# Kernel tuning notes

Hardware: AMD Instinct MI355X
Metric: run time of the kernel (lower is better)

The kernel has to match this reference:

```python
import jax, jax.numpy as jnp
import numpy as np

B, C, H, D, W = 1, 32, 32, 32, 32   # batch, channels, 3D grid
M1 = M2 = M3 = 16                   # fourier modes kept per dim
KS = 3                              # spatial attention kernel size
MEM = 5                             # memory slots
EPS = 1e-5
N = H * D * W


def _gelu(x):
    return jax.nn.gelu(x, approximate=False)  # torch exact GELU


def _gn(x):
    # GroupNorm(1, C) without affine: normalize over (C,H,D,W) per sample
    mu = jnp.mean(x, axis=(1, 2, 3, 4), keepdims=True)
    var = jnp.var(x, axis=(1, 2, 3, 4), keepdims=True)
    return (x - mu) * jax.lax.rsqrt(var + EPS)


def _spectral_conv(x, wr, wi):
    # classic 3D FNO spectral conv: keep low modes (4 corner blocks in dims H,D; low block in rfft dim W)
    xf = jnp.fft.rfftn(x, axes=(2, 3, 4))                 # (B,C,H,D,W//2+1) complex64
    w = wr + 1j * wi                                      # (4,Cin,Cout,M1,M2,M3)
    of = jnp.zeros((x.shape[0], C, H, D, W // 2 + 1), xf.dtype)
    corners = [(slice(0, M1), slice(0, M2)), (slice(H - M1, H), slice(0, M2)),
               (slice(0, M1), slice(D - M2, D)), (slice(H - M1, H), slice(D - M2, D))]
    for i, (s1, s2) in enumerate(corners):
        of = of.at[:, :, s1, s2, :M3].set(
            jnp.einsum('bixyz,ioxyz->boxyz', xf[:, :, s1, s2, :M3], w[i]))
    return jnp.fft.irfftn(of, s=(H, D, W), axes=(2, 3, 4))


def _forward(x, t, prev_memory, w_spec_r, w_spec_i, norm1_g, norm1_b,
             mlp_w1, mlp_b1, mlp_w2, mlp_b2, tin_gw, tin_gb, tin_bw, tin_bb,
             q_w, q_b, k_w, k_b, v_w, v_b, mem_key, mem_value,
             gate_w, gate_b, gru_wih, gru_whh, gru_bih, gru_bhh):
    skip1 = x
    skip2 = _gelu(x)
    # spectral conv -> GroupNorm(affine) + residual -> gelu
    h = _spectral_conv(x, w_spec_r, w_spec_i)
    h = _gelu(_gn(h) * norm1_g[None, :, None, None, None]
              + norm1_b[None, :, None, None, None] + skip1)
    # pointwise Conv1d MLP over channels
    hf = h.reshape(B, C, N)
    u = _gelu(jnp.einsum('oc,bcn->bon', mlp_w1, hf) + mlp_b1[None, :, None])
    hf = jnp.einsum('oc,bcn->bon', mlp_w2, u) + mlp_b2[None, :, None]
    h = hf.reshape(B, C, H, D, W)
    # time-conditioned instance norm: gamma/beta from 1x1 conv over t (B,C)
    gamma = (jnp.einsum('oc,bc->bo', tin_gw, t) + tin_gb)[:, :, None, None, None]
    beta = (jnp.einsum('oc,bc->bo', tin_bw, t) + tin_bb)[:, :, None, None, None]
    h = gamma * _gn(h) + beta
    # ---- spatial attention with memory ----
    pad = KS // 2
    xp = jnp.pad(h, ((0, 0), (0, 0), (pad, pad), (pad, pad), (pad, pad)))
    # 3D unfold: (B,C,27,N) patches via 27 shifted views
    patches = jnp.stack([xp[:, :, i:i + H, j:j + D, l:l + W]
                         for i in range(KS) for j in range(KS) for l in range(KS)],
                        axis=2).reshape(B, C, KS ** 3, N)
    hf = h.reshape(B, C, N)
    q = jnp.einsum('oc,bcn->bon', q_w, hf) + q_b[None, :, None]              # (B,C,N)
    k_sp = jnp.einsum('oc,bcmn->bomn', k_w, patches) + k_b[None, :, None, None]
    v_sp = jnp.einsum('oc,bcmn->bomn', v_w, patches) + v_b[None, :, None, None]
    mem_k = jnp.broadcast_to(mem_key[None, :, :, None], (B, C, MEM, N))
    mem_v = jnp.broadcast_to(mem_value[None, :, :, None], (B, C, MEM, N))
    k = jnp.concatenate([mem_k, k_sp], axis=2)                               # (B,C,32,N)
    v = jnp.concatenate([mem_v, v_sp], axis=2)
    attn = jax.nn.softmax(q[:, :, None, :] * k / jnp.sqrt(jnp.float32(C)), axis=2)
    out = jnp.sum(attn * v, axis=2)                                          # (B,C,N)
    cat = jnp.concatenate([hf, out], axis=1)                                 # (B,2C,N)
    gate = jax.nn.sigmoid(jnp.einsum('oc,bcn->bon', gate_w, cat) + gate_b[None, :, None])
    out = gate * out + (1.0 - gate) * hf
    out = out.reshape(B, C, H, D, W)
    # GRUCell memory update from spatially pooled features
    m_in = jnp.mean(out, axis=(2, 3, 4))                                     # (B,C)
    gi = m_in @ gru_wih.T + gru_bih
    gh = prev_memory @ gru_whh.T + gru_bhh
    ir, iz, inn = jnp.split(gi, 3, axis=1)
    hr, hz, hn = jnp.split(gh, 3, axis=1)
    r = jax.nn.sigmoid(ir + hr)
    z = jax.nn.sigmoid(iz + hz)
    n = jnp.tanh(inn + r * hn)
    new_memory = (1.0 - z) * n + z * prev_memory                             # (B,C)
    return out + skip2, new_memory


def setup_inputs():
    key = jax.random.key(0)
    ks = jax.random.split(key, 20)
    def rn(k, shape, s):
        return jax.random.normal(k, shape, jnp.float32) * s
    spec_scale = 1.0 / (C * C)
    return dict(
        x=jax.random.normal(ks[0], (B, C, H, D, W), jnp.float32),
        t=jax.random.normal(ks[1], (B, C), jnp.float32),
        prev_memory=jnp.zeros((B, C), jnp.float32),
        w_spec_r=rn(ks[2], (4, C, C, M1, M2, M3), spec_scale),
        w_spec_i=rn(ks[3], (4, C, C, M1, M2, M3), spec_scale),
        norm1_g=jnp.ones((C,), jnp.float32),
        norm1_b=jnp.zeros((C,), jnp.float32),
        mlp_w1=rn(ks[4], (C // 2, C), 0.1), mlp_b1=jnp.zeros((C // 2,), jnp.float32),
        mlp_w2=rn(ks[5], (C, C // 2), 0.1), mlp_b2=jnp.zeros((C,), jnp.float32),
        tin_gw=rn(ks[6], (C, C), 0.1), tin_gb=jnp.ones((C,), jnp.float32),
        tin_bw=rn(ks[7], (C, C), 0.1), tin_bb=jnp.zeros((C,), jnp.float32),
        q_w=rn(ks[8], (C, C), 0.1), q_b=jnp.zeros((C,), jnp.float32),
        k_w=rn(ks[9], (C, C), 0.1), k_b=jnp.zeros((C,), jnp.float32),
        v_w=rn(ks[10], (C, C), 0.1), v_b=jnp.zeros((C,), jnp.float32),
        mem_key=jax.random.normal(ks[11], (C, MEM), jnp.float32),
        mem_value=jax.random.normal(ks[12], (C, MEM), jnp.float32),
        gate_w=rn(ks[13], (C, 2 * C), 0.1), gate_b=jnp.zeros((C,), jnp.float32),
        gru_wih=rn(ks[14], (3 * C, C), 0.1), gru_whh=rn(ks[15], (3 * C, C), 0.1),
        gru_bih=jnp.zeros((3 * C,), jnp.float32), gru_bhh=jnp.zeros((3 * C,), jnp.float32),
    )


def reference(x, t, prev_memory, w_spec_r, w_spec_i, norm1_g, norm1_b,
              mlp_w1, mlp_b1, mlp_w2, mlp_b2, tin_gw, tin_gb, tin_bw, tin_bb,
              q_w, q_b, k_w, k_b, v_w, v_b, mem_key, mem_value,
              gate_w, gate_b, gru_wih, gru_whh, gru_bih, gru_bhh):
    return _forward(x, t, prev_memory, w_spec_r, w_spec_i, norm1_g, norm1_b,
                    mlp_w1, mlp_b1, mlp_w2, mlp_b2, tin_gw, tin_gb, tin_bw, tin_bb,
                    q_w, q_b, k_w, k_b, v_w, v_b, mem_key, mem_value,
                    gate_w, gate_b, gru_wih, gru_whh, gru_bih, gru_bhh)
```

## Files before the change

### kernel.cpp

```cpp
#include <hip/hip_runtime.h>
#include <hip/hip_bf16.h>
#include <math.h>

#define NSP 32768
#define NZ 17

__device__ __forceinline__ float geluf(float x){
    return 0.5f * x * (1.0f + erff(x * 0.70710678118654752f));
}
__device__ __forceinline__ float sigmoidf_(float x){
    return 1.0f / (1.0f + __expf(-x));
}


__global__ void k_fwd(const float* __restrict__ x, float* __restrict__ Br, float* __restrict__ Bi){
    __shared__ float tile[32*33];
    __shared__ float ar[544], ai[544];
    __shared__ float ct[32], st[32];
    int b = blockIdx.x, t = threadIdx.x;
    if (t < 32){ float ang = 6.283185307179586477f * (float)t / 32.0f; ct[t] = cosf(ang); st[t] = sinf(ang); }
    const float* src = x + b * 1024;
    for (int j = t; j < 1024; j += 256) tile[(j & 31) * 33 + (j >> 5)] = src[j];
    __syncthreads();
    for (int idx = t; idx < 544; idx += 256){
        int d = idx / 17, z = idx - d * 17;
        float sr = 0.f, si = 0.f;
        #pragma unroll
        for (int w = 0; w < 32; ++w){
            int a = (z * w) & 31;
            float v = tile[w * 33 + d];
            sr += v * ct[a];
            si -= v * st[a];
        }
        ar[idx] = sr; ai[idx] = si;
    }
    __syncthreads();
    for (int idx = t; idx < 544; idx += 256){
        int kd = idx / 17, z = idx - kd * 17;
        float sr = 0.f, si = 0.f;
        #pragma unroll
        for (int d = 0; d < 32; ++d){
            int a = (kd * d) & 31;
            float c = ct[a], s = st[a];
            float vr = ar[d * 17 + z], vi = ai[d * 17 + z];
            sr += vr * c + vi * s;
            si += vi * c - vr * s;
        }
        Br[b * 544 + idx] = sr; Bi[b * 544 + idx] = si;
    }
}

__global__ void k_fft_h(const float* __restrict__ Br, const float* __restrict__ Bi,
                        float* __restrict__ Ar, float* __restrict__ Ai){
    __shared__ float ir[544], ii[544];
    __shared__ float ct[32], st[32];
    int b = blockIdx.x, t = threadIdx.x;
    int c = b >> 5, d = b & 31;
    if (t < 32){ float ang = 6.283185307179586477f * (float)t / 32.0f; ct[t] = cosf(ang); st[t] = sinf(ang); }
    for (int j = t; j < 544; j += 256){
        int h = j / 17, z = j - h * 17;
        int g = ((c * 32 + h) * 32 + d) * NZ + z;
        ir[j] = Br[g]; ii[j] = Bi[g];
    }
    __syncthreads();
    for (int idx = t; idx < 544; idx += 256){
        int kh = idx / 17, z = idx - kh * 17;
        float sr = 0.f, si = 0.f;
        #pragma unroll
        for (int h = 0; h < 32; ++h){
            int a = (kh * h) & 31;
            float c2 = ct[a], s2 = st[a];
            float vr = ir[h * 17 + z], vi = ii[h * 17 + z];
            sr += vr * c2 + vi * s2;
            si += vi * c2 - vr * s2;
        }
        int g = ((c * 32 + kh) * 32 + d) * NZ + z;
        Ar[g] = sr; Ai[g] = si;
    }
}

__global__ void k_modemul(const float* __restrict__ Xr, const float* __restrict__ Xi,
                          const float* __restrict__ Wr, const float* __restrict__ Wi,
                          float* __restrict__ Or, float* __restrict__ Oi){
    int b = blockIdx.x;
    int q = b & 3;
    int o = (b >> 2) & 31;
    int corner = b >> 7;
    int t = threadIdx.x;
    int m = q * 1024 + t * 4;
    int xm = m >> 8, ym = (m >> 4) & 15, zm = m & 15;
    int xg = xm + ((corner & 1) << 4);
    int y  = ym + ((corner >> 1) << 4);
    if (t < 128){
        int xl = t >> 5;
        int arr = (t >> 4) & 1;
        int yl = t & 15;
        int xgz = q * 4 + xl + ((corner & 1) << 4);
        int yz = yl + ((corner >> 1) << 4);
        int g = ((o * 32 + xgz) * 32 + yz) * NZ + 16;
        if (arr == 0) Or[g] = 0.f; else Oi[g] = 0.f;
    }
    size_t xoff = (size_t)(xg * 32 + y) * NZ + zm;
    const float* wr = Wr + (size_t)((corner * 32) * 32 + o) * 4096 + m;
    const float* wi = Wi + (size_t)((corner * 32) * 32 + o) * 4096 + m;
    float ar0=0.f, ar1=0.f, ar2=0.f, ar3=0.f;
    float ai0=0.f, ai1=0.f, ai2=0.f, ai3=0.f;
    #pragma unroll 4
    for (int i = 0; i < 32; ++i){
        float4 w4r = *(const float4*)(wr + (size_t)i * 131072);
        float4 w4i = *(const float4*)(wi + (size_t)i * 131072);
        const float* pxr = Xr + (size_t)i * 17408 + xoff;
        const float* pxi = Xi + (size_t)i * 17408 + xoff;
        float xr0 = pxr[0], xr1 = pxr[1], xr2 = pxr[2], xr3 = pxr[3];
        float xi0 = pxi[0], xi1 = pxi[1], xi2 = pxi[2], xi3 = pxi[3];
        ar0 += w4r.x * xr0 - w4i.x * xi0;  ai0 += w4r.x * xi0 + w4i.x * xr0;
        ar1 += w4r.y * xr1 - w4i.y * xi1;  ai1 += w4r.y * xi1 + w4i.y * xr1;
        ar2 += w4r.z * xr2 - w4i.z * xi2;  ai2 += w4r.z * xi2 + w4i.z * xr2;
        ar3 += w4r.w * xr3 - w4i.w * xi3;  ai3 += w4r.w * xi3 + w4i.w * xr3;
    }
    int g = ((o * 32 + xg) * 32 + y) * NZ + zm;
    Or[g + 0] = ar0; Or[g + 1] = ar1; Or[g + 2] = ar2; Or[g + 3] = ar3;
    Oi[g + 0] = ai0; Oi[g + 1] = ai1; Oi[g + 2] = ai2; Oi[g + 3] = ai3;
}

__global__ void k_ifft_h(const float* __restrict__ Br, const float* __restrict__ Bi,
                         float* __restrict__ Ar, float* __restrict__ Ai){
    __shared__ float ir[544], ii[544];
    __shared__ float ct[32], st[32];
    int b = blockIdx.x, t = threadIdx.x;
    int c = b >> 5, y = b & 31;
    if (t < 32){ float ang = 6.283185307179586477f * (float)t / 32.0f; ct[t] = cosf(ang); st[t] = sinf(ang); }
    for (int j = t; j < 544; j += 256){
        int xk = j / 17, z = j - xk * 17;
        int g = ((c * 32 + xk) * 32 + y) * NZ + z;
        ir[j] = Br[g]; ii[j] = Bi[g];
    }
    __syncthreads();
    for (int idx = t; idx < 544; idx += 256){
        int h = idx / 17, z = idx - h * 17;
        float sr = 0.f, si = 0.f;
        #pragma unroll
        for (int k = 0; k < 32; ++k){
            int a = (k * h) & 31;
            float c2 = ct[a], s2 = st[a];
            float vr = ir[k * 17 + z], vi = ii[k * 17 + z];
            sr += vr * c2 - vi * s2;
            si += vr * s2 + vi * c2;
        }
        int g = ((c * 32 + h) * 32 + y) * NZ + z;
        Ar[g] = sr; Ai[g] = si;
    }
}

__global__ void k_inv(const float* __restrict__ Ar, const float* __restrict__ Ai,
                      float* __restrict__ spec,
                      float* __restrict__ psum, float* __restrict__ psq){
    __shared__ float ir[544], ii[544];
    __shared__ float cr[544], ci[544];
    __shared__ float ct[32], st[32];
    __shared__ float ls[256], lq[256];
    int b = blockIdx.x, t = threadIdx.x;
    if (t < 32){ float ang = 6.283185307179586477f * (float)t / 32.0f; ct[t] = cosf(ang); st[t] = sinf(ang); }
    const float* pr = Ar + b * 544;
    const float* pi = Ai + b * 544;
    for (int j = t; j < 544; j += 256){ ir[j] = pr[j]; ii[j] = pi[j]; }
    __syncthreads();
    for (int idx = t; idx < 544; idx += 256){
        int d = idx / 17, z = idx - d * 17;
        float sr = 0.f, si = 0.f;
        #pragma unroll
        for (int k = 0; k < 32; ++k){
            int a = (k * d) & 31;
            float c2 = ct[a], s2 = st[a];
            float vr = ir[k * 17 + z], vi = ii[k * 17 + z];
            sr += vr * c2 - vi * s2;
            si += vr * s2 + vi * c2;
        }
        cr[idx] = sr; ci[idx] = si;
    }
    __syncthreads();
    const float inv = 1.0f / 32768.0f;
    float s_loc = 0.f, q_loc = 0.f;
    for (int idx = t; idx < 1024; idx += 256){
        int d = idx >> 5, w = idx & 31;
        float s = cr[d * 17 + 0] + ((w & 1) ? -cr[d * 17 + 16] : cr[d * 17 + 16]);
        #pragma unroll
        for (int z = 1; z < 16; ++z){
            int a = (z * w) & 31;
            s += 2.0f * (cr[d * 17 + z] * ct[a] - ci[d * 17 + z] * st[a]);
        }
        s *= inv;
        spec[b * 1024 + idx] = s;
        s_loc += s; q_loc += s * s;
    }
    ls[t] = s_loc; lq[t] = q_loc; __syncthreads();
    for (int off = 128; off > 0; off >>= 1){
        if (t < off){ ls[t] += ls[t + off]; lq[t] += lq[t + off]; }
        __syncthreads();
    }
    if (t == 0){ psum[b] = ls[0]; psq[b] = lq[0]; }
}


__global__ void k_finalize1(const float* __restrict__ psum, const float* __restrict__ psq,
                            int n, float* __restrict__ red){
    __shared__ float ls[256], lq[256];
    int t = threadIdx.x;
    float s = 0.f, q = 0.f;
    for (int j = t; j < n; j += 256){ s += psum[j]; q += psq[j]; }
    ls[t] = s; lq[t] = q; __syncthreads();
    for (int off = 128; off > 0; off >>= 1){
        if (t < off){ ls[t] += ls[t + off]; lq[t] += lq[t + off]; }
        __syncthreads();
    }
    if (t == 0){
        float mu = ls[0] * (1.0f / 1048576.0f);
        float var = lq[0] * (1.0f / 1048576.0f) - mu * mu;
        red[0] = mu; red[1] = rsqrtf(var + 1e-5f);
    }
}

__global__ void k_finalize2(const float* __restrict__ psum, const float* __restrict__ psq,
                            int n, const float* __restrict__ tin,
                            const float* __restrict__ tgw, const float* __restrict__ tgb,
                            const float* __restrict__ tbw, const float* __restrict__ tbb,
                            float* __restrict__ red){
    __shared__ float ls[256], lq[256];
    int t = threadIdx.x;
    float s = 0.f, q = 0.f;
    for (int j = t; j < n; j += 256){ s += psum[j]; q += psq[j]; }
    ls[t] = s; lq[t] = q; __syncthreads();
    for (int off = 128; off > 0; off >>= 1){
        if (t < off){ ls[t] += ls[t + off]; lq[t] += lq[t + off]; }
        __syncthreads();
    }
    if (t == 0){
        float mu = ls[0] * (1.0f / 1048576.0f);
        float var = lq[0] * (1.0f / 1048576.0f) - mu * mu;
        red[2] = mu; red[3] = rsqrtf(var + 1e-5f);
    }
    if (t < 64){
        int o = t & 31;
        const float* w = (t < 32) ? tgw : tbw;
        const float* bi = (t < 32) ? tgb : tbb;
        float a = bi[o];
        #pragma unroll
        for (int c = 0; c < 32; ++c) a += w[o * 32 + c] * tin[c];
        red[(t < 32 ? 16 : 48) + o] = a;
    }
}

__global__ void k_mlp(const float* __restrict__ spec, const float* __restrict__ x,
                      const float* __restrict__ n1g, const float* __restrict__ n1b,
                      const float* __restrict__ red,
                      const float* __restrict__ w1, const float* __restrict__ b1,
                      const float* __restrict__ w2, const float* __restrict__ b2,
                      float* __restrict__ h2,
                      float* __restrict__ psum, float* __restrict__ psq){
    __shared__ float W1[512], W2[512], B1[16], B2[32], GG[32], BB[32];
    __shared__ float ls[256], lq[256];
    int t = threadIdx.x;
    for (int j = t; j < 512; j += 256){ W1[j] = w1[j]; W2[j] = w2[j]; }
    if (t < 16) B1[t] = b1[t];
    if (t < 32){ B2[t] = b2[t]; GG[t] = n1g[t]; BB[t] = n1b[t]; }
    __syncthreads();
    float mu = red[0], rs = red[1];
    int n = blockIdx.x * 256 + t;
    float hv[32];
    #pragma unroll
    for (int c = 0; c < 32; ++c){
        float v = (spec[c * NSP + n] - mu) * rs * GG[c] + BB[c] + x[c * NSP + n];
        hv[c] = geluf(v);
    }
    float u[16];
    #pragma unroll
    for (int o = 0; o < 16; ++o){
        float a = B1[o];
        #pragma unroll
        for (int c = 0; c < 32; ++c) a += W1[o * 32 + c] * hv[c];
        u[o] = geluf(a);
    }
    float s_loc = 0.f, q_loc = 0.f;
    #pragma unroll
    for (int o = 0; o < 32; ++o){
        float a = B2[o];
        #pragma unroll
        for (int c = 0; c < 16; ++c) a += W2[o * 16 + c] * u[c];
        h2[o * NSP + n] = a;
        s_loc += a; q_loc += a * a;
    }
    ls[t] = s_loc; lq[t] = q_loc; __syncthreads();
    for (int off = 128; off > 0; off >>= 1){
        if (t < off){ ls[t] += ls[t + off]; lq[t] += lq[t + off]; }
        __syncthreads();
    }
    if (t == 0){ psum[blockIdx.x] = ls[0]; psq[blockIdx.x] = lq[0]; }
}

__global__ void k_qkv(const float* __restrict__ h2, const float* __restrict__ red,
                      const float* __restrict__ qw, const float* __restrict__ qb,
                      const float* __restrict__ kw, const float* __restrict__ vw,
                      float* __restrict__ h3, float* __restrict__ Q,
                      float* __restrict__ KH, float* __restrict__ VH){
    __shared__ float QW[1024], KW[1024], VW[1024], GA[32], BE[32], QB[32];
    int t = threadIdx.x;
    for (int j = t; j < 1024; j += 256){ QW[j] = qw[j]; KW[j] = kw[j]; VW[j] = vw[j]; }
    if (t < 32){ GA[t] = red[16 + t]; BE[t] = red[48 + t]; QB[t] = qb[t]; }
    __syncthreads();
    float mu = red[2], rs = red[3];
    int n = blockIdx.x * 256 + t;
    float hv[32];
    #pragma unroll
    for (int c = 0; c < 32; ++c){
        float v = GA[c] * ((h2[c * NSP + n] - mu) * rs) + BE[c];
        hv[c] = v;
        h3[c * NSP + n] = v;
    }
    #pragma unroll
    for (int o = 0; o < 32; ++o){
        float aq = QB[o], ak = 0.f, av = 0.f;
        #pragma unroll
        for (int c = 0; c < 32; ++c){
            float v = hv[c];
            aq += QW[o * 32 + c] * v;
            ak += KW[o * 32 + c] * v;
            av += VW[o * 32 + c] * v;
        }
        Q[o * NSP + n] = aq;
        KH[o * NSP + n] = ak;
        VH[o * NSP + n] = av;
    }
}

__global__ void k_attn(const float* __restrict__ Q, const float* __restrict__ KH,
                       const float* __restrict__ VH,
                       const float* __restrict__ kb, const float* __restrict__ vb,
                       const float* __restrict__ mk, const float* __restrict__ mv,
                       float* __restrict__ out0){
    __shared__ float KL[3][1024], VL[3][1024];
    int bid = blockIdx.x;
    int swz = (bid & 7) * 128 + (bid >> 3);
    int c = swz >> 5, h_ = swz & 31;
    int t = threadIdx.x;
    #pragma unroll
    for (int p = 0; p < 3; ++p){
        int hh = h_ - 1 + p;
        if ((unsigned)hh < 32u){
            const float* sk = KH + (c * 32 + hh) * 1024;
            const float* sv = VH + (c * 32 + hh) * 1024;
            for (int j = t; j < 1024; j += 256){ KL[p][j] = sk[j]; VL[p][j] = sv[j]; }
        }
    }
    float kbc = kb[c], vbc = vb[c];
    float mkv[5], mvv[5];
    #pragma unroll
    for (int j = 0; j < 5; ++j){ mkv[j] = mk[c * 5 + j]; mvv[j] = mv[c * 5 + j]; }
    float qv[4];
    #pragma unroll
    for (int i = 0; i < 4; ++i) qv[i] = Q[c * NSP + h_ * 1024 + i * 256 + t];
    __syncthreads();
    const float scale = 0.17677669529663688f;
    #pragma unroll
    for (int i = 0; i < 4; ++i){
        int nl = i * 256 + t;
        int d_ = nl >> 5, w_ = nl & 31;
        float q = qv[i];
        float s = 0.f, acc = 0.f;
        #pragma unroll
        for (int j = 0; j < 5; ++j){
            float e = __expf(q * mkv[j] * scale);
            s += e; acc += e * mvv[j];
        }
        int oob = 0;
        #pragma unroll
        for (int p = 0; p < 3; ++p){
            int hh = h_ - 1 + p;
            if ((unsigned)hh >= 32u){ oob += 9; continue; }
            #pragma unroll
            for (int dj = -1; dj <= 1; ++dj){
                int dd = d_ + dj;
                if ((unsigned)dd >= 32u){ oob += 3; continue; }
                int rb = dd * 32;
                #pragma unroll
                for (int dl = -1; dl <= 1; ++dl){
                    int ww = w_ + dl;
                    if ((unsigned)ww < 32u){
                        float k = kbc + KL[p][rb + ww];
                        float v = vbc + VL[p][rb + ww];
                        float e = __expf(q * k * scale);
                        s += e; acc += e * v;
                    } else oob++;
                }
            }
        }
        float eb = __expf(q * kbc * scale);
        s += (float)oob * eb; acc += (float)oob * eb * vbc;
        out0[c * NSP + h_ * 1024 + nl] = acc / s;
    }
}

__global__ void k_gate(const float* __restrict__ h3, const float* __restrict__ out0,
                       const float* __restrict__ x,
                       const float* __restrict__ gw, const float* __restrict__ gb,
                       float* __restrict__ outp, float* __restrict__ mpart){
    __shared__ float GW[2048];
    __shared__ float FT[32 * 264];
    __shared__ float PS[256];
    int t = threadIdx.x;
    for (int j = t; j < 2048; j += 256) GW[j] = gw[j];
    int n = blockIdx.x * 256 + t;
    float hv[32], ov[32];
    #pragma unroll
    for (int c = 0; c < 32; ++c){ hv[c] = h3[c * NSP + n]; ov[c] = out0[c * NSP + n]; }
    __syncthreads();
    #pragma unroll
    for (int c = 0; c < 32; ++c){
        float g = gb[c];
        #pragma unroll
        for (int cc = 0; cc < 32; ++cc){
            g += GW[c * 64 + cc] * hv[cc] + GW[c * 64 + 32 + cc] * ov[cc];
        }
        g = sigmoidf_(g);
        float fin = g * ov[c] + (1.0f - g) * hv[c];
        FT[c * 264 + t] = fin;
        outp[c * NSP + n] = fin + geluf(x[c * NSP + n]);
    }
    __syncthreads();
    {
        int c8 = t >> 3, seg = t & 7;
        float s = 0.f;
        #pragma unroll
        for (int j = 0; j < 32; ++j) s += FT[c8 * 264 + seg * 32 + j];
        PS[t] = s;
    }
    __syncthreads();
    if (t < 32){
        float s = 0.f;
        #pragma unroll
        for (int j = 0; j < 8; ++j) s += PS[t * 8 + j];
        mpart[t * 128 + blockIdx.x] = s;
    }
}

__global__ void k_mred(const float* __restrict__ mpart, float* __restrict__ red){
    __shared__ float ls[128];
    int c = blockIdx.x, t = threadIdx.x;
    ls[t] = mpart[c * 128 + t];
    __syncthreads();
    for (int off = 64; off > 0; off >>= 1){
        if (t < off) ls[t] += ls[t + off];
        __syncthreads();
    }
    if (t == 0) red[128 + c] = ls[0] * (1.0f / 32768.0f);
}

__global__ void k_gru(const float* __restrict__ red, const float* __restrict__ pm,
                      const float* __restrict__ wih, const float* __restrict__ whh,
                      const float* __restrict__ bih, const float* __restrict__ bhh,
                      float* __restrict__ outp){
    __shared__ float m_in[32], gi[96], gh[96];
    int t = threadIdx.x;
    if (t < 32) m_in[t] = red[128 + t];
    __syncthreads();
    if (t < 96){
        float a = bih[t], b2 = bhh[t];
        #pragma unroll
        for (int cc = 0; cc < 32; ++cc){
            a += wih[t * 32 + cc] * m_in[cc];
            b2 += whh[t * 32 + cc] * pm[cc];
        }
        gi[t] = a; gh[t] = b2;
    }
    __syncthreads();
    if (t < 32){
        float r = sigmoidf_(gi[t] + gh[t]);
        float z = sigmoidf_(gi[32 + t] + gh[32 + t]);
        float nn = tanhf(gi[64 + t] + r * gh[64 + t]);
        float nm = (1.0f - z) * nn + z * pm[t];
        outp[1048576 + t] = nm;
    }
}

extern "C" void kernel_launch(void* const* d_in, const int* in_sizes, int n_in,
                              void* d_out, int out_size, void* d_ws, size_t ws_size,
                              hipStream_t stream){
    const float* x   = (const float*)d_in[0];
    const float* tin = (const float*)d_in[1];
    const float* pm  = (const float*)d_in[2];
    const float* wsr = (const float*)d_in[3];
    const float* wsi = (const float*)d_in[4];
    const float* n1g = (const float*)d_in[5];
    const float* n1b = (const float*)d_in[6];
    const float* mw1 = (const float*)d_in[7];
    const float* mb1 = (const float*)d_in[8];
    const float* mw2 = (const float*)d_in[9];
    const float* mb2 = (const float*)d_in[10];
    const float* tgw = (const float*)d_in[11];
    const float* tgb = (const float*)d_in[12];
    const float* tbw = (const float*)d_in[13];
    const float* tbb = (const float*)d_in[14];
    const float* qw  = (const float*)d_in[15];
    const float* qb  = (const float*)d_in[16];
    const float* kw  = (const float*)d_in[17];
    const float* kb  = (const float*)d_in[18];
    const float* vw  = (const float*)d_in[19];
    const float* vb  = (const float*)d_in[20];
    const float* mk  = (const float*)d_in[21];
    const float* mv  = (const float*)d_in[22];
    const float* gw  = (const float*)d_in[23];
    const float* gb  = (const float*)d_in[24];
    const float* wih = (const float*)d_in[25];
    const float* whh = (const float*)d_in[26];
    const float* bih = (const float*)d_in[27];
    const float* bhh = (const float*)d_in[28];

    float* ws = (float*)d_ws;
    float* Ar   = ws + 0;
    float* Ai   = ws + 557056;
    float* Br   = ws + 1114112;
    float* Bi   = ws + 1671168;
    float* spec = ws + 2228224;
    float* h1   = ws + 3276800;
    float* h2   = ws + 4325376;
    float* h3   = ws + 5373952;
    float* red  = ws + 6422528;
    float* psum = ws + 6422784;
    float* psq  = ws + 6423808;
    float* Qb   = Br;
    float* KHb  = spec;
    float* VHb  = h1;
    float* out0 = Ar;
    float* mpart = h2;

    float* outp = (float*)d_out;

    k_fwd    <<<1024, 256, 0, stream>>>(x, Br, Bi);
    k_fft_h  <<<1024, 256, 0, stream>>>(Br, Bi, Ar, Ai);
    k_modemul<<<512, 256, 0, stream>>>(Ar, Ai, wsr, wsi, Br, Bi);
    k_ifft_h <<<1024, 256, 0, stream>>>(Br, Bi, Ar, Ai);
    k_inv    <<<1024, 256, 0, stream>>>(Ar, Ai, spec, psum, psq);
    k_finalize1<<<1, 256, 0, stream>>>(psum, psq, 1024, red);
    k_mlp    <<<128, 256, 0, stream>>>(spec, x, n1g, n1b, red, mw1, mb1, mw2, mb2, h2, psum, psq);
    k_finalize2<<<1, 256, 0, stream>>>(psum, psq, 128, tin, tgw, tgb, tbw, tbb, red);
    k_qkv    <<<128, 256, 0, stream>>>(h2, red, qw, qb, kw, vw, h3, Qb, KHb, VHb);
    k_attn   <<<1024, 256, 0, stream>>>(Qb, KHb, VHb, kb, vb, mk, mv, out0);
    k_gate   <<<128, 256, 0, stream>>>(h3, out0, x, gw, gb, outp, mpart);
    k_mred   <<<32, 128, 0, stream>>>(mpart, red);
    k_gru    <<<1, 128, 0, stream>>>(red, pm, wih, whh, bih, bhh, outp);
}
```

Measured before the change: 191.4 us.

## Fold reduction finalize kernels into consumers and prefetch spectral weights into cache

Removes the finalize1, finalize2 and mred launches. Each consumer block (k_mlp, k_qkv, k_gru) now redundantly reduces the partial sums itself, which saves launch and serialization overhead at the cost of duplicated small reductions. It also adds dummy reads of the spectral weights (wsr, wsi) in the first two FFT kernels, meant to warm L2/MALL before k_modemul. This adds extra memory traffic in those kernels, and the results are written into the psum/psq buffers, which k_inv later overwrites.

```diff
diff --git a/kernel.cpp b/kernel.cpp
--- a/kernel.cpp
+++ b/kernel.cpp
@@ -13,12 +13,22 @@
 }
 
 
-__global__ void k_fwd(const float* __restrict__ x, float* __restrict__ Br, float* __restrict__ Bi){
+__global__ void k_fwd(const float* __restrict__ x, float* __restrict__ Br, float* __restrict__ Bi,
+                      const float* __restrict__ wpref, float* __restrict__ dummy){
     __shared__ float tile[32*33];
     __shared__ float ar[544], ai[544];
     __shared__ float ct[32], st[32];
     int b = blockIdx.x, t = threadIdx.x;
     if (t < 32){ float ang = 6.283185307179586477f * (float)t / 32.0f; ct[t] = cosf(ang); st[t] = sinf(ang); }
+    {
+        const float4* wp = (const float4*)(wpref) + (size_t)b * 4096;
+        float acc = 0.f;
+        for (int j = t; j < 4096; j += 256){
+            float4 v = wp[j];
+            acc += v.x + v.y + v.z + v.w;
+        }
+        dummy[b] = acc;
+    }
     const float* src = x + b * 1024;
     for (int j = t; j < 1024; j += 256) tile[(j & 31) * 33 + (j >> 5)] = src[j];
     __syncthreads();
@@ -51,12 +61,22 @@
 }
 
 __global__ void k_fft_h(const float* __restrict__ Br, const float* __restrict__ Bi,
-                        float* __restrict__ Ar, float* __restrict__ Ai){
+                        float* __restrict__ Ar, float* __restrict__ Ai,
+                        const float* __restrict__ wpref, float* __restrict__ dummy){
     __shared__ float ir[544], ii[544];
     __shared__ float ct[32], st[32];
     int b = blockIdx.x, t = threadIdx.x;
     int c = b >> 5, d = b & 31;
     if (t < 32){ float ang = 6.283185307179586477f * (float)t / 32.0f; ct[t] = cosf(ang); st[t] = sinf(ang); }
+    {
+        const float4* wp = (const float4*)(wpref) + (size_t)b * 4096;
+        float acc = 0.f;
+        for (int j = t; j < 4096; j += 256){
+            float4 v = wp[j];
+            acc += v.x + v.y + v.z + v.w;
+        }
+        dummy[b] = acc;
+    }
     for (int j = t; j < 544; j += 256){
         int h = j / 17, z = j - h * 17;
         int g = ((c * 32 + h) * 32 + d) * NZ + z;
@@ -202,69 +222,30 @@
 }
 
 
-__global__ void k_finalize1(const float* __restrict__ psum, const float* __restrict__ psq,
-                            int n, float* __restrict__ red){
-    __shared__ float ls[256], lq[256];
-    int t = threadIdx.x;
-    float s = 0.f, q = 0.f;
-    for (int j = t; j < n; j += 256){ s += psum[j]; q += psq[j]; }
-    ls[t] = s; lq[t] = q; __syncthreads();
-    for (int off = 128; off > 0; off >>= 1){
-        if (t < off){ ls[t] += ls[t + off]; lq[t] += lq[t + off]; }
-        __syncthreads();
-    }
-    if (t == 0){
-        float mu = ls[0] * (1.0f / 1048576.0f);
-        float var = lq[0] * (1.0f / 1048576.0f) - mu * mu;
-        red[0] = mu; red[1] = rsqrtf(var + 1e-5f);
-    }
-}
-
-__global__ void k_finalize2(const float* __restrict__ psum, const float* __restrict__ psq,
-                            int n, const float* __restrict__ tin,
-                            const float* __restrict__ tgw, const float* __restrict__ tgb,
-                            const float* __restrict__ tbw, const float* __restrict__ tbb,
-                            float* __restrict__ red){
-    __shared__ float ls[256], lq[256];
-    int t = threadIdx.x;
-    float s = 0.f, q = 0.f;
-    for (int j = t; j < n; j += 256){ s += psum[j]; q += psq[j]; }
-    ls[t] = s; lq[t] = q; __syncthreads();
-    for (int off = 128; off > 0; off >>= 1){
-        if (t < off){ ls[t] += ls[t + off]; lq[t] += lq[t + off]; }
-        __syncthreads();
-    }
-    if (t == 0){
-        float mu = ls[0] * (1.0f / 1048576.0f);
-        float var = lq[0] * (1.0f / 1048576.0f) - mu * mu;
-        red[2] = mu; red[3] = rsqrtf(var + 1e-5f);
-    }
-    if (t < 64){
-        int o = t & 31;
-        const float* w = (t < 32) ? tgw : tbw;
-        const float* bi = (t < 32) ? tgb : tbb;
-        float a = bi[o];
-        #pragma unroll
-        for (int c = 0; c < 32; ++c) a += w[o * 32 + c] * tin[c];
-        red[(t < 32 ? 16 : 48) + o] = a;
-    }
-}
-
 __global__ void k_mlp(const float* __restrict__ spec, const float* __restrict__ x,
                       const float* __restrict__ n1g, const float* __restrict__ n1b,
-                      const float* __restrict__ red,
+                      const float* __restrict__ psum, const float* __restrict__ psq,
                       const float* __restrict__ w1, const float* __restrict__ b1,
                       const float* __restrict__ w2, const float* __restrict__ b2,
                       float* __restrict__ h2,
-                      float* __restrict__ psum, float* __restrict__ psq){
+                      float* __restrict__ psum2, float* __restrict__ psq2){
     __shared__ float W1[512], W2[512], B1[16], B2[32], GG[32], BB[32];
     __shared__ float ls[256], lq[256];
     int t = threadIdx.x;
     for (int j = t; j < 512; j += 256){ W1[j] = w1[j]; W2[j] = w2[j]; }
     if (t < 16) B1[t] = b1[t];
     if (t < 32){ B2[t] = b2[t]; GG[t] = n1g[t]; BB[t] = n1b[t]; }
-    __syncthreads();
-    float mu = red[0], rs = red[1];
+    float s0 = 0.f, q0 = 0.f;
+    for (int j = t; j < 1024; j += 256){ s0 += psum[j]; q0 += psq[j]; }
+    ls[t] = s0; lq[t] = q0; __syncthreads();
+    for (int off = 128; off > 0; off >>= 1){
+        if (t < off){ ls[t] += ls[t + off]; lq[t] += lq[t + off]; }
+        __syncthreads();
+    }
+    float mu = ls[0] * (1.0f / 1048576.0f);
+    float var = lq[0] * (1.0f / 1048576.0f) - mu * mu;
+    float rs = rsqrtf(var + 1e-5f);
+    __syncthreads();
     int n = blockIdx.x * 256 + t;
     float hv[32];
     #pragma unroll
@@ -294,20 +275,44 @@
         if (t < off){ ls[t] += ls[t + off]; lq[t] += lq[t + off]; }
         __syncthreads();
     }
-    if (t == 0){ psum[blockIdx.x] = ls[0]; psq[blockIdx.x] = lq[0]; }
-}
-
-__global__ void k_qkv(const float* __restrict__ h2, const float* __restrict__ red,
+    if (t == 0){ psum2[blockIdx.x] = ls[0]; psq2[blockIdx.x] = lq[0]; }
+}
+
+__global__ void k_qkv(const float* __restrict__ h2,
+                      const float* __restrict__ psum2, const float* __restrict__ psq2,
+                      const float* __restrict__ tin,
+                      const float* __restrict__ tgw, const float* __restrict__ tgb,
+                      const float* __restrict__ tbw, const float* __restrict__ tbb,
                       const float* __restrict__ qw, const float* __restrict__ qb,
                       const float* __restrict__ kw, const float* __restrict__ vw,
                       float* __restrict__ h3, float* __restrict__ Q,
                       float* __restrict__ KH, float* __restrict__ VH){
     __shared__ float QW[1024], KW[1024], VW[1024], GA[32], BE[32], QB[32];
+    __shared__ float ls[256], lq[256];
     int t = threadIdx.x;
     for (int j = t; j < 1024; j += 256){ QW[j] = qw[j]; KW[j] = kw[j]; VW[j] = vw[j]; }
-    if (t < 32){ GA[t] = red[16 + t]; BE[t] = red[48 + t]; QB[t] = qb[t]; }
-    __syncthreads();
-    float mu = red[2], rs = red[3];
+    if (t < 32) QB[t] = qb[t];
+    ls[t] = (t < 128) ? psum2[t] : 0.f;
+    lq[t] = (t < 128) ? psq2[t] : 0.f;
+    __syncthreads();
+    for (int off = 128; off > 0; off >>= 1){
+        if (t < off){ ls[t] += ls[t + off]; lq[t] += lq[t + off]; }
+        __syncthreads();
+    }
+    float mu = ls[0] * (1.0f / 1048576.0f);
+    float var = lq[0] * (1.0f / 1048576.0f) - mu * mu;
+    float rs = rsqrtf(var + 1e-5f);
+    __syncthreads();
+    if (t < 64){
+        int o = t & 31;
+        const float* w = (t < 32) ? tgw : tbw;
+        const float* bi = (t < 32) ? tgb : tbb;
+        float a = bi[o];
+        #pragma unroll
+        for (int c = 0; c < 32; ++c) a += w[o * 32 + c] * tin[c];
+        if (t < 32) GA[o] = a; else BE[o] = a;
+    }
+    __syncthreads();
     int n = blockIdx.x * 256 + t;
     float hv[32];
     #pragma unroll
@@ -442,25 +447,27 @@
     }
 }
 
-__global__ void k_mred(const float* __restrict__ mpart, float* __restrict__ red){
-    __shared__ float ls[128];
-    int c = blockIdx.x, t = threadIdx.x;
-    ls[t] = mpart[c * 128 + t];
-    __syncthreads();
-    for (int off = 64; off > 0; off >>= 1){
-        if (t < off) ls[t] += ls[t + off];
-        __syncthreads();
-    }
-    if (t == 0) red[128 + c] = ls[0] * (1.0f / 32768.0f);
-}
-
-__global__ void k_gru(const float* __restrict__ red, const float* __restrict__ pm,
+__global__ void k_gru(const float* __restrict__ mpart, const float* __restrict__ pm,
                       const float* __restrict__ wih, const float* __restrict__ whh,
                       const float* __restrict__ bih, const float* __restrict__ bhh,
                       float* __restrict__ outp){
+    __shared__ float PS[256];
     __shared__ float m_in[32], gi[96], gh[96];
     int t = threadIdx.x;
-    if (t < 32) m_in[t] = red[128 + t];
+    {
+        int c = t >> 3, seg = t & 7;
+        float s = 0.f;
+        #pragma unroll
+        for (int j = 0; j < 16; ++j) s += mpart[c * 128 + seg * 16 + j];
+        PS[t] = s;
+    }
+    __syncthreads();
+    if (t < 32){
+        float a = 0.f;
+        #pragma unroll
+        for (int j = 0; j < 8; ++j) a += PS[t * 8 + j];
+        m_in[t] = a * (1.0f / 32768.0f);
+    }
     __syncthreads();
     if (t < 96){
         float a = bih[t], b2 = bhh[t];
@@ -515,36 +522,36 @@
     const float* bhh = (const float*)d_in[28];
 
     float* ws = (float*)d_ws;
-    float* Ar   = ws + 0;
-    float* Ai   = ws + 557056;
-    float* Br   = ws + 1114112;
-    float* Bi   = ws + 1671168;
-    float* spec = ws + 2228224;
-    float* h1   = ws + 3276800;
-    float* h2   = ws + 4325376;
-    float* h3   = ws + 5373952;
-    float* red  = ws + 6422528;
-    float* psum = ws + 6422784;
-    float* psq  = ws + 6423808;
-    float* Qb   = Br;
-    float* KHb  = spec;
-    float* VHb  = h1;
-    float* out0 = Ar;
+    float* Ar    = ws + 0;
+    float* Ai    = ws + 557056;
+    float* Br    = ws + 1114112;
+    float* Bi    = ws + 1671168;
+    float* spec  = ws + 2228224;
+    float* h1    = ws + 3276800;
+    float* h2    = ws + 4325376;
+    float* h3    = ws + 5373952;
+    float* red   = ws + 6422528;
+    float* psum  = ws + 6422784;
+    float* psq   = ws + 6423808;
+    float* psum2 = ws + 6424832;
+    float* psq2  = ws + 6425856;
+    (void)red;
+    float* Qb    = Br;
+    float* KHb   = spec;
+    float* VHb   = h1;
+    float* out0  = Ar;
     float* mpart = h2;
 
     float* outp = (float*)d_out;
 
-    k_fwd    <<<1024, 256, 0, stream>>>(x, Br, Bi);
-    k_fft_h  <<<1024, 256, 0, stream>>>(Br, Bi, Ar, Ai);
+    k_fwd    <<<1024, 256, 0, stream>>>(x, Br, Bi, wsr, psum);
+    k_fft_h  <<<1024, 256, 0, stream>>>(Br, Bi, Ar, Ai, wsi, psq);
     k_modemul<<<512, 256, 0, stream>>>(Ar, Ai, wsr, wsi, Br, Bi);
     k_ifft_h <<<1024, 256, 0, stream>>>(Br, Bi, Ar, Ai);
     k_inv    <<<1024, 256, 0, stream>>>(Ar, Ai, spec, psum, psq);
-    k_finalize1<<<1, 256, 0, stream>>>(psum, psq, 1024, red);
-    k_mlp    <<<128, 256, 0, stream>>>(spec, x, n1g, n1b, red, mw1, mb1, mw2, mb2, h2, psum, psq);
-    k_finalize2<<<1, 256, 0, stream>>>(psum, psq, 128, tin, tgw, tgb, tbw, tbb, red);
-    k_qkv    <<<128, 256, 0, stream>>>(h2, red, qw, qb, kw, vw, h3, Qb, KHb, VHb);
+    k_mlp    <<<128, 256, 0, stream>>>(spec, x, n1g, n1b, psum, psq, mw1, mb1, mw2, mb2, h2, psum2, psq2);
+    k_qkv    <<<128, 256, 0, stream>>>(h2, psum2, psq2, tin, tgw, tgb, tbw, tbb, qw, qb, kw, vw, h3, Qb, KHb, VHb);
     k_attn   <<<1024, 256, 0, stream>>>(Qb, KHb, VHb, kb, vb, mk, mv, out0);
     k_gate   <<<128, 256, 0, stream>>>(h3, out0, x, gw, gb, outp, mpart);
-    k_mred   <<<32, 128, 0, stream>>>(mpart, red);
-    k_gru    <<<1, 128, 0, stream>>>(red, pm, wih, whh, bih, bhh, outp);
-}
+    k_gru    <<<1, 256, 0, stream>>>(mpart, pm, wih, whh, bih, bhh, outp);
+}
```

After: 207.0 us. 1.08x slower.
